# Performance work log

Hardware: AMD Instinct MI355X
Metric: run time of the kernel (lower is better)

The kernel has to match this reference:

```python
import jax, jax.numpy as jnp
import numpy as np


def setup_inputs() -> dict:
    key = jax.random.key(0)
    k1, k2, k3, k4 = jax.random.split(key, 4)
    B, T_dec, T_enc, H2 = 8, 64, 512, 512  # H2 = 2*hiddenSize
    encoderOutput = jax.random.normal(k1, (B, T_enc, H2), dtype=jnp.float32)
    decoderInput = jax.random.normal(k2, (B, T_dec, H2), dtype=jnp.float32)
    # fc: Linear(4H -> 2H); torch weight layout [out, in] = [2H, 4H]
    W = jax.random.normal(k3, (H2, 2 * H2), dtype=jnp.float32) * (1.0 / np.sqrt(2 * H2))
    b = jax.random.normal(k4, (H2,), dtype=jnp.float32) * 0.01
    return {"encoderOutput": encoderOutput, "decoderInput": decoderInput, "W": W, "b": b}


def reference(encoderOutput, decoderInput, W, b):
    # Original: for each (i, j), fc(cat(dec[:,i], enc[:,j])) then log_softmax over
    # the FEATURE dim (dim=1 of the flattened [-1, 2H] tensor), then
    # context[:, i] = sum_j log_softmax(...) * enc[:, j].
    H2 = encoderOutput.shape[-1]
    W_dec = W[:, :H2]   # columns multiplying the decoder half of the concat
    W_enc = W[:, H2:]   # columns multiplying the encoder half
    dec_part = jnp.einsum('bid,od->bio', decoderInput, W_dec)   # [B, T_dec, 2H]
    enc_part = jnp.einsum('bjd,od->bjo', encoderOutput, W_enc)  # [B, T_enc, 2H]
    logits = dec_part[:, :, None, :] + enc_part[:, None, :, :] + b  # [B, T_dec, T_enc, 2H]
    alpha = jax.nn.log_softmax(logits, axis=-1)  # softmax over feature dim, as in source
    context = jnp.einsum('bijd,bjd->bid', alpha, encoderOutput)  # [B, T_dec, 2H]
    return context
```

## Files before the change

kernel.cpp:

```cpp
#include <hip/hip_runtime.h>


namespace {
constexpr int kH  = 512;
constexpr int kTD = 64;
constexpr int kTE = 512;
constexpr int kB  = 8;
constexpr int kRD = kB * kTD;
constexpr int kRE = kB * kTE;
}

typedef __attribute__((ext_vector_type(8))) short short8;
typedef __attribute__((ext_vector_type(4))) float floatx4;

__device__ __forceinline__ unsigned short f2bf(float x) {
    unsigned u = __float_as_uint(x);
    u += 0x7fffu + ((u >> 16) & 1u);
    return (unsigned short)(u >> 16);
}
__device__ __forceinline__ float bf2f(unsigned short h) {
    return __uint_as_float(((unsigned)h) << 16);
}
__device__ __forceinline__ size_t fragTile(int rtile, int kt) {
    return ((size_t)rtile * 16 + kt) * 512;
}
__device__ __forceinline__ short8 pack8(float4 a, float4 b) {
    short8 r;
    r[0] = (short)f2bf(a.x); r[1] = (short)f2bf(a.y);
    r[2] = (short)f2bf(a.z); r[3] = (short)f2bf(a.w);
    r[4] = (short)f2bf(b.x); r[5] = (short)f2bf(b.y);
    r[6] = (short)f2bf(b.z); r[7] = (short)f2bf(b.w);
    return r;
}

__global__ __launch_bounds__(256) void fused_cast(
    const float* __restrict__ W, const float* __restrict__ dec,
    const float* __restrict__ enc,
    unsigned short* __restrict__ Wd_f, unsigned short* __restrict__ We_f,
    unsigned short* __restrict__ dec_f,
    unsigned short* __restrict__ enc_f, unsigned short* __restrict__ encT_f,
    float* __restrict__ S12)
{
    const int blk = blockIdx.x, t = threadIdx.x;
    const int w = t >> 6, l = t & 63;
    const int lr = l & 15, lc = l >> 4;
    if (blk < 256) {
        const int gw = blk * 4 + w;
        const int sel = gw >> 9, rem = gw & 511;
        const int ot = rem >> 4, kt = rem & 15;
        const int o = ot * 16 + lr;
        const float* src = W + (size_t)o * 1024 + sel * 512 + kt * 32 + lc * 8;
        const float4 v0 = *(const float4*)src;
        const float4 v1 = *(const float4*)(src + 4);
        unsigned short* dst = (sel ? We_f : Wd_f) + fragTile(ot, kt) + l * 8;
        *(short8*)dst = pack8(v0, v1);
        if (blk < 32) S12[blk * 256 + t] = 0.f;
    } else if (blk < 384) {
        const int gw = (blk - 256) * 4 + w;
        const int rt = gw >> 4, kt = gw & 15;
        const int r = rt * 16 + lr;
        const float* src = dec + (size_t)r * kH + kt * 32 + lc * 8;
        const float4 v0 = *(const float4*)src;
        const float4 v1 = *(const float4*)(src + 4);
        *(short8*)(dec_f + fragTile(rt, kt) + l * 8) = pack8(v0, v1);
    } else {
        __shared__ unsigned short s[64][36];
        const int e = blk - 384;
        const int kt = e & 15, jt = (e >> 4) & 7, b = e >> 7;
        const int j0 = jt * 64, d0 = kt * 32;
        const int jl = w * 16 + lr;
        const float* src = enc + ((size_t)(b * kTE + j0 + jl)) * kH + d0 + lc * 8;
        const float4 v0 = *(const float4*)src;
        const float4 v1 = *(const float4*)(src + 4);
        const short8 p = pack8(v0, v1);
        *(short8*)(enc_f + fragTile(b * 32 + jt * 4 + w, kt) + l * 8) = p;
#pragma unroll
        for (int i = 0; i < 8; ++i) s[jl][lc * 8 + i] = (unsigned short)p[i];
        __syncthreads();
        const int dt = w >> 1, jc = w & 1;
        const int dl = dt * 16 + lr;
        const int j8 = jc * 32 + lc * 8;
        short8 v;
#pragma unroll
        for (int i = 0; i < 8; ++i) v[i] = (short)s[j8 + i][dl];
        *(short8*)(encT_f + fragTile(b * 32 + kt * 2 + dt, jt * 2 + jc) + l * 8) = v;
    }
}

__global__ __launch_bounds__(256) void gemm1(
    const unsigned short* __restrict__ enc_f,
    const unsigned short* __restrict__ dec_f,
    const unsigned short* __restrict__ Wd_f,
    const unsigned short* __restrict__ We_f,
    const float* __restrict__ bias,
    const float* __restrict__ enc,
    unsigned short* __restrict__ part_bf, unsigned short* __restrict__ uv_f,
    float* __restrict__ S12)
{
    __shared__ float As[64][68];
    __shared__ float r1[16][68];
    __shared__ float r2[16][68];
    const int tile = blockIdx.x;
    const int ns = tile & 7, ms = tile >> 3;
    const int t = threadIdx.x, w = t >> 6, l = t & 63;
    const int qm = w >> 1, qn = w & 1;
    const bool isenc = (ms >= 8);
    const unsigned short* A = isenc ? enc_f : dec_f;
    const unsigned short* Bw = isenc ? We_f : Wd_f;
    const int art = (isenc ? (ms - 8) : ms) * 4 + qm * 2;
    const int brt = ns * 4 + qn * 2;

    floatx4 acc[2][2];
#pragma unroll
    for (int m = 0; m < 2; ++m)
#pragma unroll
        for (int n = 0; n < 2; ++n) acc[m][n] = (floatx4){0.f, 0.f, 0.f, 0.f};

    for (int kt = 0; kt < 16; ++kt) {
        short8 af[2], bfr[2];
#pragma unroll
        for (int m = 0; m < 2; ++m)
            af[m] = *(const short8*)(A + fragTile(art + m, kt) + l * 8);
#pragma unroll
        for (int n = 0; n < 2; ++n)
            bfr[n] = *(const short8*)(Bw + fragTile(brt + n, kt) + l * 8);
#pragma unroll
        for (int m = 0; m < 2; ++m)
#pragma unroll
            for (int n = 0; n < 2; ++n)
                acc[m][n] = __builtin_amdgcn_mfma_f32_16x16x32_bf16(af[m], bfr[n], acc[m][n], 0, 0, 0);
    }

    const int lr = l & 15, lq = l >> 4;
#pragma unroll
    for (int m = 0; m < 2; ++m)
#pragma unroll
        for (int n = 0; n < 2; ++n)
#pragma unroll
            for (int r = 0; r < 4; ++r)
                As[qm * 32 + m * 16 + lq * 4 + r][qn * 32 + n * 16 + lr] = acc[m][n][r];
    __syncthreads();

    const int rowbase = ms * 64, colbase = ns * 64;
    if (!isenc) {
#pragma unroll
        for (int h = 0; h < 2; ++h) {
            const int a = h * 256 + t;
            const int row = a >> 3, cc = (a & 7) * 8;
            const float4 v0 = *(const float4*)&As[row][cc];
            const float4 v1 = *(const float4*)&As[row][cc + 4];
            *(short8*)(part_bf + (size_t)(rowbase + row) * kH + colbase + cc) = pack8(v0, v1);
        }
    }
#pragma unroll
    for (int h = 0; h < 2; ++h) {
        const int s = h * 256 + t;
        const int rt = s >> 7, kc = (s >> 6) & 1, fl = s & 63;
        const int row = rt * 16 + (fl & 15);
        const int col = kc * 32 + (fl >> 4) * 8;
        const float4 v0 = *(const float4*)&As[row][col];
        const float4 v1 = *(const float4*)&As[row][col + 4];
        float4 b0 = make_float4(0.f, 0.f, 0.f, 0.f), b1 = b0;
        if (isenc) {
            b0 = *(const float4*)(bias + colbase + col);
            b1 = *(const float4*)(bias + colbase + col + 4);
        }
        short8 u;
        u[0] = (short)f2bf(__expf(v0.x + b0.x));
        u[1] = (short)f2bf(__expf(v0.y + b0.y));
        u[2] = (short)f2bf(__expf(v0.z + b0.z));
        u[3] = (short)f2bf(__expf(v0.w + b0.w));
        u[4] = (short)f2bf(__expf(v1.x + b1.x));
        u[5] = (short)f2bf(__expf(v1.y + b1.y));
        u[6] = (short)f2bf(__expf(v1.z + b1.z));
        u[7] = (short)f2bf(__expf(v1.w + b1.w));
        *(short8*)(uv_f + fragTile(ms * 4 + rt, ns * 2 + kc) + fl * 8) = u;
    }
    if (isenc) {
        const int b = (ms - 8) >> 3;
        const int jbase = ((ms - 8) & 7) * 64;
        const int o4 = (t & 15) * 4, jg = t >> 4;
        float4 s1p = make_float4(0.f, 0.f, 0.f, 0.f);
        float4 s2p = make_float4(0.f, 0.f, 0.f, 0.f);
#pragma unroll
        for (int jj = 0; jj < 4; ++jj) {
            const int j = jg * 4 + jj;
            const float4 ev = *(const float4*)(
                enc + ((size_t)(b * kTE + jbase + j)) * kH + colbase + o4);
            const float4 pv = *(const float4*)&As[j][o4];
            s1p.x += ev.x; s1p.y += ev.y; s1p.z += ev.z; s1p.w += ev.w;
            s2p.x = fmaf(pv.x, ev.x, s2p.x);
            s2p.y = fmaf(pv.y, ev.y, s2p.y);
            s2p.z = fmaf(pv.z, ev.z, s2p.z);
            s2p.w = fmaf(pv.w, ev.w, s2p.w);
        }
        *(float4*)&r1[jg][o4] = s1p;
        *(float4*)&r2[jg][o4] = s2p;
        __syncthreads();
        if (t < 64) {
            float a1 = 0.f, a2 = 0.f;
#pragma unroll
            for (int g = 0; g < 16; ++g) { a1 += r1[g][t]; a2 += r2[g][t]; }
            atomicAdd(&S12[b * kH + colbase + t], a1);
            atomicAdd(&S12[4096 + b * kH + colbase + t], a2);
        }
    }
}

__global__ __launch_bounds__(256) void lse_k(
    const unsigned short* __restrict__ uv_f, unsigned short* __restrict__ lse_f)
{
    __shared__ float red[4][16][68];
    const int blk = blockIdx.x, t = threadIdx.x;
    const int b = blk >> 5, rem = blk & 31;
    const int it = rem >> 3, jt = rem & 7;
    const int w = t >> 6, l = t & 63;
    const int art = b * 4 + it;
    const int vrt0 = 32 + b * 32 + jt * 4;

    floatx4 acc[4];
#pragma unroll
    for (int n = 0; n < 4; ++n) acc[n] = (floatx4){0.f, 0.f, 0.f, 0.f};
#pragma unroll
    for (int kk = 0; kk < 4; ++kk) {
        const int kt = w * 4 + kk;
        const short8 af = *(const short8*)(uv_f + fragTile(art, kt) + l * 8);
#pragma unroll
        for (int n = 0; n < 4; ++n)
            acc[n] = __builtin_amdgcn_mfma_f32_16x16x32_bf16(
                af, *(const short8*)(uv_f + fragTile(vrt0 + n, kt) + l * 8), acc[n], 0, 0, 0);
    }
    const int lr = l & 15, lq = l >> 4;
#pragma unroll
    for (int n = 0; n < 4; ++n)
#pragma unroll
        for (int r = 0; r < 4; ++r)
            red[w][lq * 4 + r][n * 16 + lr] = acc[n][r];
    __syncthreads();
    const int s = t >> 1, h = t & 1;
    const int kc = s >> 6, fl = s & 63;
    const int i = fl & 15;
    const int j = kc * 32 + (fl >> 4) * 8 + h * 4;
    float4 sum = *(const float4*)&red[0][i][j];
    const float4 s1 = *(const float4*)&red[1][i][j];
    const float4 s2 = *(const float4*)&red[2][i][j];
    const float4 s3 = *(const float4*)&red[3][i][j];
    sum.x += s1.x + s2.x + s3.x; sum.y += s1.y + s2.y + s3.y;
    sum.z += s1.z + s2.z + s3.z; sum.w += s1.w + s2.w + s3.w;
    ushort4 o;
    o.x = f2bf(__logf(sum.x)); o.y = f2bf(__logf(sum.y));
    o.z = f2bf(__logf(sum.z)); o.w = f2bf(__logf(sum.w));
    *(ushort4*)(lse_f + fragTile(b * 4 + it, jt * 2 + kc) + fl * 8 + h * 4) = o;
}

__global__ __launch_bounds__(256) void final_k(
    const unsigned short* __restrict__ lse_f,
    const unsigned short* __restrict__ encT_f,
    const unsigned short* __restrict__ part_bf,
    const float* __restrict__ bias,
    const float* __restrict__ S12,
    float* __restrict__ out)
{
    __shared__ float red[4][16][68];
    const int blk = blockIdx.x, t = threadIdx.x;
    const int b = blk >> 5, rem = blk & 31;
    const int it = rem >> 3, dt = rem & 7;
    const int w = t >> 6, l = t & 63;
    const int art = b * 4 + it;
    const int brt0 = b * 32 + dt * 4;

    floatx4 acc[4];
#pragma unroll
    for (int n = 0; n < 4; ++n) acc[n] = (floatx4){0.f, 0.f, 0.f, 0.f};
#pragma unroll
    for (int kk = 0; kk < 4; ++kk) {
        const int kt = w * 4 + kk;
        const short8 af = *(const short8*)(lse_f + fragTile(art, kt) + l * 8);
#pragma unroll
        for (int n = 0; n < 4; ++n)
            acc[n] = __builtin_amdgcn_mfma_f32_16x16x32_bf16(
                af, *(const short8*)(encT_f + fragTile(brt0 + n, kt) + l * 8), acc[n], 0, 0, 0);
    }
    const int lr = l & 15, lq = l >> 4;
#pragma unroll
    for (int n = 0; n < 4; ++n)
#pragma unroll
        for (int r = 0; r < 4; ++r)
            red[w][lq * 4 + r][n * 16 + lr] = acc[n][r];
    __syncthreads();
    const int i = t >> 4, d0 = (t & 15) * 4;
    float4 m = *(const float4*)&red[0][i][d0];
    const float4 m1 = *(const float4*)&red[1][i][d0];
    const float4 m2 = *(const float4*)&red[2][i][d0];
    const float4 m3 = *(const float4*)&red[3][i][d0];
    m.x += m1.x + m2.x + m3.x; m.y += m1.y + m2.y + m3.y;
    m.z += m1.z + m2.z + m3.z; m.w += m1.w + m2.w + m3.w;

    const int gd = dt * 64 + d0;
    const float4 s1 = *(const float4*)(S12 + b * kH + gd);
    const float4 s2 = *(const float4*)(S12 + 4096 + b * kH + gd);
    const float4 bi = *(const float4*)(bias + gd);
    const int row = b * kTD + it * 16 + i;
    const ushort4 dp = *(const ushort4*)(part_bf + (size_t)row * kH + gd);
    float4 o;
    o.x = fmaf(bf2f(dp.x) + bi.x, s1.x, s2.x) - m.x;
    o.y = fmaf(bf2f(dp.y) + bi.y, s1.y, s2.y) - m.y;
    o.z = fmaf(bf2f(dp.z) + bi.z, s1.z, s2.z) - m.z;
    o.w = fmaf(bf2f(dp.w) + bi.w, s1.w, s2.w) - m.w;
    *(float4*)(out + (size_t)row * kH + gd) = o;
}

extern "C" void kernel_launch(void* const* d_in, const int* in_sizes, int n_in,
                              void* d_out, int out_size, void* d_ws, size_t ws_size,
                              hipStream_t stream)
{
    (void)in_sizes; (void)n_in; (void)out_size; (void)ws_size;
    const float* enc  = (const float*)d_in[0];
    const float* dec  = (const float*)d_in[1];
    const float* W    = (const float*)d_in[2];
    const float* bias = (const float*)d_in[3];
    float* out = (float*)d_out;

    char* base = (char*)d_ws;
    unsigned short* part_bf = (unsigned short*)(base);
    unsigned short* uv_f    = (unsigned short*)(base + 4718592);
    unsigned short* enc_f   = (unsigned short*)(base + 9437184);
    unsigned short* encT_f  = (unsigned short*)(base + 13631488);
    unsigned short* dec_f   = (unsigned short*)(base + 17825792);
    unsigned short* Wd_f    = (unsigned short*)(base + 18350080);
    unsigned short* We_f    = (unsigned short*)(base + 18874368);
    unsigned short* lse_f   = (unsigned short*)(base + 19398656);
    float*          S12     = (float*)(base + 19922944);

    fused_cast<<<1408, 256, 0, stream>>>(W, dec, enc, Wd_f, We_f, dec_f,
                                         enc_f, encT_f, S12);
    gemm1<<<576, 256, 0, stream>>>(enc_f, dec_f, Wd_f, We_f, bias, enc,
                                   part_bf, uv_f, S12);
    lse_k<<<256, 256, 0, stream>>>(uv_f, lse_f);
    final_k<<<256, 256, 0, stream>>>(lse_f, encT_f, part_bf, bias, S12, out);
}
```

Measured before the change: 91.87 us.

## Merge four kernels into one cooperative persistent kernel with grid syncs

Replaces the four separate launches (cast, gemm1, lse, final) with a single cooperative kernel of 288 blocks that loops over the original block indices and separates the phases with grid-wide syncs. This removes three kernel launch gaps and their tail effects. The cost is fewer blocks than the original grids (1408 and 576), so each block does several units serially. The last two phases use only 256 of the 288 blocks, and grid.sync adds its own overhead.

Result: slower. 208.2 us (+126.7%).

```diff
diff --git a/kernel.cpp b/kernel.cpp
--- a/kernel.cpp
+++ b/kernel.cpp
@@ -1,4 +1,7 @@
 #include <hip/hip_runtime.h>
+#include <hip/hip_cooperative_groups.h>
+
+namespace cg = cooperative_groups;
 
 
 namespace {
@@ -7,7 +10,6 @@
 constexpr int kTE = 512;
 constexpr int kB  = 8;
 constexpr int kRD = kB * kTD;
-constexpr int kRE = kB * kTE;
 }
 
 typedef __attribute__((ext_vector_type(8))) short short8;
@@ -33,281 +35,271 @@
     return r;
 }
 
-__global__ __launch_bounds__(256) void fused_cast(
+__global__ void __launch_bounds__(256) mega(
     const float* __restrict__ W, const float* __restrict__ dec,
-    const float* __restrict__ enc,
+    const float* __restrict__ enc, const float* __restrict__ bias,
     unsigned short* __restrict__ Wd_f, unsigned short* __restrict__ We_f,
     unsigned short* __restrict__ dec_f,
     unsigned short* __restrict__ enc_f, unsigned short* __restrict__ encT_f,
-    float* __restrict__ S12)
+    unsigned short* __restrict__ part_bf, unsigned short* __restrict__ uv_f,
+    unsigned short* __restrict__ lse_f,
+    float* __restrict__ S12, float* __restrict__ out)
 {
-    const int blk = blockIdx.x, t = threadIdx.x;
-    const int w = t >> 6, l = t & 63;
+    cg::grid_group grid = cg::this_grid();
+    const int t = threadIdx.x, w = t >> 6, l = t & 63;
     const int lr = l & 15, lc = l >> 4;
-    if (blk < 256) {
-        const int gw = blk * 4 + w;
-        const int sel = gw >> 9, rem = gw & 511;
-        const int ot = rem >> 4, kt = rem & 15;
-        const int o = ot * 16 + lr;
-        const float* src = W + (size_t)o * 1024 + sel * 512 + kt * 32 + lc * 8;
-        const float4 v0 = *(const float4*)src;
-        const float4 v1 = *(const float4*)(src + 4);
-        unsigned short* dst = (sel ? We_f : Wd_f) + fragTile(ot, kt) + l * 8;
-        *(short8*)dst = pack8(v0, v1);
-        if (blk < 32) S12[blk * 256 + t] = 0.f;
-    } else if (blk < 384) {
-        const int gw = (blk - 256) * 4 + w;
-        const int rt = gw >> 4, kt = gw & 15;
-        const int r = rt * 16 + lr;
-        const float* src = dec + (size_t)r * kH + kt * 32 + lc * 8;
-        const float4 v0 = *(const float4*)src;
-        const float4 v1 = *(const float4*)(src + 4);
-        *(short8*)(dec_f + fragTile(rt, kt) + l * 8) = pack8(v0, v1);
-    } else {
-        __shared__ unsigned short s[64][36];
-        const int e = blk - 384;
-        const int kt = e & 15, jt = (e >> 4) & 7, b = e >> 7;
-        const int j0 = jt * 64, d0 = kt * 32;
-        const int jl = w * 16 + lr;
-        const float* src = enc + ((size_t)(b * kTE + j0 + jl)) * kH + d0 + lc * 8;
-        const float4 v0 = *(const float4*)src;
-        const float4 v1 = *(const float4*)(src + 4);
-        const short8 p = pack8(v0, v1);
-        *(short8*)(enc_f + fragTile(b * 32 + jt * 4 + w, kt) + l * 8) = p;
-#pragma unroll
-        for (int i = 0; i < 8; ++i) s[jl][lc * 8 + i] = (unsigned short)p[i];
-        __syncthreads();
-        const int dt = w >> 1, jc = w & 1;
-        const int dl = dt * 16 + lr;
-        const int j8 = jc * 32 + lc * 8;
-        short8 v;
-#pragma unroll
-        for (int i = 0; i < 8; ++i) v[i] = (short)s[j8 + i][dl];
-        *(short8*)(encT_f + fragTile(b * 32 + kt * 2 + dt, jt * 2 + jc) + l * 8) = v;
-    }
-}
-
-__global__ __launch_bounds__(256) void gemm1(
-    const unsigned short* __restrict__ enc_f,
-    const unsigned short* __restrict__ dec_f,
-    const unsigned short* __restrict__ Wd_f,
-    const unsigned short* __restrict__ We_f,
-    const float* __restrict__ bias,
-    const float* __restrict__ enc,
-    unsigned short* __restrict__ part_bf, unsigned short* __restrict__ uv_f,
-    float* __restrict__ S12)
-{
-    __shared__ float As[64][68];
-    __shared__ float r1[16][68];
-    __shared__ float r2[16][68];
-    const int tile = blockIdx.x;
-    const int ns = tile & 7, ms = tile >> 3;
-    const int t = threadIdx.x, w = t >> 6, l = t & 63;
-    const int qm = w >> 1, qn = w & 1;
-    const bool isenc = (ms >= 8);
-    const unsigned short* A = isenc ? enc_f : dec_f;
-    const unsigned short* Bw = isenc ? We_f : Wd_f;
-    const int art = (isenc ? (ms - 8) : ms) * 4 + qm * 2;
-    const int brt = ns * 4 + qn * 2;
-
-    floatx4 acc[2][2];
-#pragma unroll
-    for (int m = 0; m < 2; ++m)
-#pragma unroll
-        for (int n = 0; n < 2; ++n) acc[m][n] = (floatx4){0.f, 0.f, 0.f, 0.f};
-
-    for (int kt = 0; kt < 16; ++kt) {
-        short8 af[2], bfr[2];
-#pragma unroll
-        for (int m = 0; m < 2; ++m)
-            af[m] = *(const short8*)(A + fragTile(art + m, kt) + l * 8);
-#pragma unroll
-        for (int n = 0; n < 2; ++n)
-            bfr[n] = *(const short8*)(Bw + fragTile(brt + n, kt) + l * 8);
-#pragma unroll
-        for (int m = 0; m < 2; ++m)
-#pragma unroll
-            for (int n = 0; n < 2; ++n)
-                acc[m][n] = __builtin_amdgcn_mfma_f32_16x16x32_bf16(af[m], bfr[n], acc[m][n], 0, 0, 0);
-    }
-
-    const int lr = l & 15, lq = l >> 4;
-#pragma unroll
-    for (int m = 0; m < 2; ++m)
-#pragma unroll
-        for (int n = 0; n < 2; ++n)
-#pragma unroll
-            for (int r = 0; r < 4; ++r)
-                As[qm * 32 + m * 16 + lq * 4 + r][qn * 32 + n * 16 + lr] = acc[m][n][r];
-    __syncthreads();
-
-    const int rowbase = ms * 64, colbase = ns * 64;
-    if (!isenc) {
-#pragma unroll
-        for (int h = 0; h < 2; ++h) {
-            const int a = h * 256 + t;
-            const int row = a >> 3, cc = (a & 7) * 8;
-            const float4 v0 = *(const float4*)&As[row][cc];
-            const float4 v1 = *(const float4*)&As[row][cc + 4];
-            *(short8*)(part_bf + (size_t)(rowbase + row) * kH + colbase + cc) = pack8(v0, v1);
+    __shared__ __align__(16) char smem[26112];
+
+    for (int u = blockIdx.x; u < 1408; u += gridDim.x) {
+        if (u < 256) {
+            const int gw = u * 4 + w;
+            const int sel = gw >> 9, rem = gw & 511;
+            const int ot = rem >> 4, kt = rem & 15;
+            const int o = ot * 16 + lr;
+            const float* src = W + (size_t)o * 1024 + sel * 512 + kt * 32 + lc * 8;
+            const float4 v0 = *(const float4*)src;
+            const float4 v1 = *(const float4*)(src + 4);
+            unsigned short* dst = (sel ? We_f : Wd_f) + fragTile(ot, kt) + l * 8;
+            *(short8*)dst = pack8(v0, v1);
+            if (u < 32) S12[u * 256 + t] = 0.f;
+        } else if (u < 384) {
+            const int gw = (u - 256) * 4 + w;
+            const int rt = gw >> 4, kt = gw & 15;
+            const int r = rt * 16 + lr;
+            const float* src = dec + (size_t)r * kH + kt * 32 + lc * 8;
+            const float4 v0 = *(const float4*)src;
+            const float4 v1 = *(const float4*)(src + 4);
+            *(short8*)(dec_f + fragTile(rt, kt) + l * 8) = pack8(v0, v1);
+        } else {
+            unsigned short (*s)[36] = (unsigned short(*)[36])smem;
+            const int e = u - 384;
+            const int kt = e & 15, jt = (e >> 4) & 7, b = e >> 7;
+            const int j0 = jt * 64, d0 = kt * 32;
+            const int jl = w * 16 + lr;
+            const float* src = enc + ((size_t)(b * kTE + j0 + jl)) * kH + d0 + lc * 8;
+            const float4 v0 = *(const float4*)src;
+            const float4 v1 = *(const float4*)(src + 4);
+            const short8 p = pack8(v0, v1);
+            *(short8*)(enc_f + fragTile(b * 32 + jt * 4 + w, kt) + l * 8) = p;
+            __syncthreads();
+#pragma unroll
+            for (int i = 0; i < 8; ++i) s[jl][lc * 8 + i] = (unsigned short)p[i];
+            __syncthreads();
+            const int dt = w >> 1, jc = w & 1;
+            const int dl = dt * 16 + lr;
+            const int j8 = jc * 32 + lc * 8;
+            short8 v;
+#pragma unroll
+            for (int i = 0; i < 8; ++i) v[i] = (short)s[j8 + i][dl];
+            *(short8*)(encT_f + fragTile(b * 32 + kt * 2 + dt, jt * 2 + jc) + l * 8) = v;
         }
     }
-#pragma unroll
-    for (int h = 0; h < 2; ++h) {
-        const int s = h * 256 + t;
-        const int rt = s >> 7, kc = (s >> 6) & 1, fl = s & 63;
-        const int row = rt * 16 + (fl & 15);
-        const int col = kc * 32 + (fl >> 4) * 8;
-        const float4 v0 = *(const float4*)&As[row][col];
-        const float4 v1 = *(const float4*)&As[row][col + 4];
-        float4 b0 = make_float4(0.f, 0.f, 0.f, 0.f), b1 = b0;
-        if (isenc) {
-            b0 = *(const float4*)(bias + colbase + col);
-            b1 = *(const float4*)(bias + colbase + col + 4);
-        }
-        short8 u;
-        u[0] = (short)f2bf(__expf(v0.x + b0.x));
-        u[1] = (short)f2bf(__expf(v0.y + b0.y));
-        u[2] = (short)f2bf(__expf(v0.z + b0.z));
-        u[3] = (short)f2bf(__expf(v0.w + b0.w));
-        u[4] = (short)f2bf(__expf(v1.x + b1.x));
-        u[5] = (short)f2bf(__expf(v1.y + b1.y));
-        u[6] = (short)f2bf(__expf(v1.z + b1.z));
-        u[7] = (short)f2bf(__expf(v1.w + b1.w));
-        *(short8*)(uv_f + fragTile(ms * 4 + rt, ns * 2 + kc) + fl * 8) = u;
-    }
-    if (isenc) {
-        const int b = (ms - 8) >> 3;
-        const int jbase = ((ms - 8) & 7) * 64;
-        const int o4 = (t & 15) * 4, jg = t >> 4;
-        float4 s1p = make_float4(0.f, 0.f, 0.f, 0.f);
-        float4 s2p = make_float4(0.f, 0.f, 0.f, 0.f);
-#pragma unroll
-        for (int jj = 0; jj < 4; ++jj) {
-            const int j = jg * 4 + jj;
-            const float4 ev = *(const float4*)(
-                enc + ((size_t)(b * kTE + jbase + j)) * kH + colbase + o4);
-            const float4 pv = *(const float4*)&As[j][o4];
-            s1p.x += ev.x; s1p.y += ev.y; s1p.z += ev.z; s1p.w += ev.w;
-            s2p.x = fmaf(pv.x, ev.x, s2p.x);
-            s2p.y = fmaf(pv.y, ev.y, s2p.y);
-            s2p.z = fmaf(pv.z, ev.z, s2p.z);
-            s2p.w = fmaf(pv.w, ev.w, s2p.w);
-        }
-        *(float4*)&r1[jg][o4] = s1p;
-        *(float4*)&r2[jg][o4] = s2p;
-        __syncthreads();
-        if (t < 64) {
-            float a1 = 0.f, a2 = 0.f;
-#pragma unroll
-            for (int g = 0; g < 16; ++g) { a1 += r1[g][t]; a2 += r2[g][t]; }
-            atomicAdd(&S12[b * kH + colbase + t], a1);
-            atomicAdd(&S12[4096 + b * kH + colbase + t], a2);
+    grid.sync();
+
+    {
+        float (*As)[68] = (float(*)[68])smem;
+        float (*r1)[68] = (float(*)[68])(smem + 17408);
+        float (*r2)[68] = (float(*)[68])(smem + 21760);
+        const int qm = w >> 1, qn = w & 1;
+        for (int tile = blockIdx.x; tile < 576; tile += gridDim.x) {
+            const int ns = tile & 7, ms = tile >> 3;
+            const bool isenc = (ms >= 8);
+            const unsigned short* A = isenc ? enc_f : dec_f;
+            const unsigned short* Bw = isenc ? We_f : Wd_f;
+            const int art = (isenc ? (ms - 8) : ms) * 4 + qm * 2;
+            const int brt = ns * 4 + qn * 2;
+
+            floatx4 acc[2][2];
+#pragma unroll
+            for (int m = 0; m < 2; ++m)
+#pragma unroll
+                for (int n = 0; n < 2; ++n) acc[m][n] = (floatx4){0.f, 0.f, 0.f, 0.f};
+
+            for (int kt = 0; kt < 16; ++kt) {
+                short8 af[2], bfr[2];
+#pragma unroll
+                for (int m = 0; m < 2; ++m)
+                    af[m] = *(const short8*)(A + fragTile(art + m, kt) + l * 8);
+#pragma unroll
+                for (int n = 0; n < 2; ++n)
+                    bfr[n] = *(const short8*)(Bw + fragTile(brt + n, kt) + l * 8);
+#pragma unroll
+                for (int m = 0; m < 2; ++m)
+#pragma unroll
+                    for (int n = 0; n < 2; ++n)
+                        acc[m][n] = __builtin_amdgcn_mfma_f32_16x16x32_bf16(af[m], bfr[n], acc[m][n], 0, 0, 0);
+            }
+
+            __syncthreads();
+#pragma unroll
+            for (int m = 0; m < 2; ++m)
+#pragma unroll
+                for (int n = 0; n < 2; ++n)
+#pragma unroll
+                    for (int r = 0; r < 4; ++r)
+                        As[qm * 32 + m * 16 + (l >> 4) * 4 + r][qn * 32 + n * 16 + lr] = acc[m][n][r];
+            __syncthreads();
+
+            const int rowbase = ms * 64, colbase = ns * 64;
+            if (!isenc) {
+#pragma unroll
+                for (int h = 0; h < 2; ++h) {
+                    const int a = h * 256 + t;
+                    const int row = a >> 3, cc = (a & 7) * 8;
+                    const float4 v0 = *(const float4*)&As[row][cc];
+                    const float4 v1 = *(const float4*)&As[row][cc + 4];
+                    *(short8*)(part_bf + (size_t)(rowbase + row) * kH + colbase + cc) = pack8(v0, v1);
+                }
+            }
+#pragma unroll
+            for (int h = 0; h < 2; ++h) {
+                const int s = h * 256 + t;
+                const int rt = s >> 7, kc = (s >> 6) & 1, fl = s & 63;
+                const int row = rt * 16 + (fl & 15);
+                const int col = kc * 32 + (fl >> 4) * 8;
+                const float4 v0 = *(const float4*)&As[row][col];
+                const float4 v1 = *(const float4*)&As[row][col + 4];
+                float4 b0 = make_float4(0.f, 0.f, 0.f, 0.f), b1 = b0;
+                if (isenc) {
+                    b0 = *(const float4*)(bias + colbase + col);
+                    b1 = *(const float4*)(bias + colbase + col + 4);
+                }
+                short8 uu;
+                uu[0] = (short)f2bf(__expf(v0.x + b0.x));
+                uu[1] = (short)f2bf(__expf(v0.y + b0.y));
+                uu[2] = (short)f2bf(__expf(v0.z + b0.z));
+                uu[3] = (short)f2bf(__expf(v0.w + b0.w));
+                uu[4] = (short)f2bf(__expf(v1.x + b1.x));
+                uu[5] = (short)f2bf(__expf(v1.y + b1.y));
+                uu[6] = (short)f2bf(__expf(v1.z + b1.z));
+                uu[7] = (short)f2bf(__expf(v1.w + b1.w));
+                *(short8*)(uv_f + fragTile(ms * 4 + rt, ns * 2 + kc) + fl * 8) = uu;
+            }
+            if (isenc) {
+                const int b = (ms - 8) >> 3;
+                const int jbase = ((ms - 8) & 7) * 64;
+                const int o4 = (t & 15) * 4, jg = t >> 4;
+                float4 s1p = make_float4(0.f, 0.f, 0.f, 0.f);
+                float4 s2p = make_float4(0.f, 0.f, 0.f, 0.f);
+#pragma unroll
+                for (int jj = 0; jj < 4; ++jj) {
+                    const int j = jg * 4 + jj;
+                    const float4 ev = *(const float4*)(
+                        enc + ((size_t)(b * kTE + jbase + j)) * kH + colbase + o4);
+                    const float4 pv = *(const float4*)&As[j][o4];
+                    s1p.x += ev.x; s1p.y += ev.y; s1p.z += ev.z; s1p.w += ev.w;
+                    s2p.x = fmaf(pv.x, ev.x, s2p.x);
+                    s2p.y = fmaf(pv.y, ev.y, s2p.y);
+                    s2p.z = fmaf(pv.z, ev.z, s2p.z);
+                    s2p.w = fmaf(pv.w, ev.w, s2p.w);
+                }
+                *(float4*)&r1[jg][o4] = s1p;
+                *(float4*)&r2[jg][o4] = s2p;
+                __syncthreads();
+                if (t < 64) {
+                    float a1 = 0.f, a2 = 0.f;
+#pragma unroll
+                    for (int g = 0; g < 16; ++g) { a1 += r1[g][t]; a2 += r2[g][t]; }
+                    atomicAdd(&S12[b * kH + colbase + t], a1);
+                    atomicAdd(&S12[4096 + b * kH + colbase + t], a2);
+                }
+            }
         }
     }
-}
-
-__global__ __launch_bounds__(256) void lse_k(
-    const unsigned short* __restrict__ uv_f, unsigned short* __restrict__ lse_f)
-{
-    __shared__ float red[4][16][68];
-    const int blk = blockIdx.x, t = threadIdx.x;
-    const int b = blk >> 5, rem = blk & 31;
-    const int it = rem >> 3, jt = rem & 7;
-    const int w = t >> 6, l = t & 63;
-    const int art = b * 4 + it;
-    const int vrt0 = 32 + b * 32 + jt * 4;
-
-    floatx4 acc[4];
-#pragma unroll
-    for (int n = 0; n < 4; ++n) acc[n] = (floatx4){0.f, 0.f, 0.f, 0.f};
-#pragma unroll
-    for (int kk = 0; kk < 4; ++kk) {
-        const int kt = w * 4 + kk;
-        const short8 af = *(const short8*)(uv_f + fragTile(art, kt) + l * 8);
+    grid.sync();
+
+    if (blockIdx.x < 256) {
+        float (*red)[16][68] = (float(*)[16][68])smem;
+        const int blk = blockIdx.x;
+        const int b = blk >> 5, rem = blk & 31;
+        const int it = rem >> 3, jt = rem & 7;
+        const int art = b * 4 + it;
+        const int vrt0 = 32 + b * 32 + jt * 4;
+
+        floatx4 acc[4];
+#pragma unroll
+        for (int n = 0; n < 4; ++n) acc[n] = (floatx4){0.f, 0.f, 0.f, 0.f};
+#pragma unroll
+        for (int kk = 0; kk < 4; ++kk) {
+            const int kt = w * 4 + kk;
+            const short8 af = *(const short8*)(uv_f + fragTile(art, kt) + l * 8);
+#pragma unroll
+            for (int n = 0; n < 4; ++n)
+                acc[n] = __builtin_amdgcn_mfma_f32_16x16x32_bf16(
+                    af, *(const short8*)(uv_f + fragTile(vrt0 + n, kt) + l * 8), acc[n], 0, 0, 0);
+        }
+        const int lq = l >> 4;
 #pragma unroll
         for (int n = 0; n < 4; ++n)
-            acc[n] = __builtin_amdgcn_mfma_f32_16x16x32_bf16(
-                af, *(const short8*)(uv_f + fragTile(vrt0 + n, kt) + l * 8), acc[n], 0, 0, 0);
+#pragma unroll
+            for (int r = 0; r < 4; ++r)
+                red[w][lq * 4 + r][n * 16 + lr] = acc[n][r];
+        __syncthreads();
+        const int s = t >> 1, h = t & 1;
+        const int kc = s >> 6, fl = s & 63;
+        const int i = fl & 15;
+        const int j = kc * 32 + (fl >> 4) * 8 + h * 4;
+        float4 sum = *(const float4*)&red[0][i][j];
+        const float4 s1 = *(const float4*)&red[1][i][j];
+        const float4 s2 = *(const float4*)&red[2][i][j];
+        const float4 s3 = *(const float4*)&red[3][i][j];
+        sum.x += s1.x + s2.x + s3.x; sum.y += s1.y + s2.y + s3.y;
+        sum.z += s1.z + s2.z + s3.z; sum.w += s1.w + s2.w + s3.w;
+        ushort4 o;
+        o.x = f2bf(__logf(sum.x)); o.y = f2bf(__logf(sum.y));
+        o.z = f2bf(__logf(sum.z)); o.w = f2bf(__logf(sum.w));
+        *(ushort4*)(lse_f + fragTile(b * 4 + it, jt * 2 + kc) + fl * 8 + h * 4) = o;
     }
-    const int lr = l & 15, lq = l >> 4;
-#pragma unroll
-    for (int n = 0; n < 4; ++n)
-#pragma unroll
-        for (int r = 0; r < 4; ++r)
-            red[w][lq * 4 + r][n * 16 + lr] = acc[n][r];
-    __syncthreads();
-    const int s = t >> 1, h = t & 1;
-    const int kc = s >> 6, fl = s & 63;
-    const int i = fl & 15;
-    const int j = kc * 32 + (fl >> 4) * 8 + h * 4;
-    float4 sum = *(const float4*)&red[0][i][j];
-    const float4 s1 = *(const float4*)&red[1][i][j];
-    const float4 s2 = *(const float4*)&red[2][i][j];
-    const float4 s3 = *(const float4*)&red[3][i][j];
-    sum.x += s1.x + s2.x + s3.x; sum.y += s1.y + s2.y + s3.y;
-    sum.z += s1.z + s2.z + s3.z; sum.w += s1.w + s2.w + s3.w;
-    ushort4 o;
-    o.x = f2bf(__logf(sum.x)); o.y = f2bf(__logf(sum.y));
-    o.z = f2bf(__logf(sum.z)); o.w = f2bf(__logf(sum.w));
-    *(ushort4*)(lse_f + fragTile(b * 4 + it, jt * 2 + kc) + fl * 8 + h * 4) = o;
-}
-
-__global__ __launch_bounds__(256) void final_k(
-    const unsigned short* __restrict__ lse_f,
-    const unsigned short* __restrict__ encT_f,
-    const unsigned short* __restrict__ part_bf,
-    const float* __restrict__ bias,
-    const float* __restrict__ S12,
-    float* __restrict__ out)
-{
-    __shared__ float red[4][16][68];
-    const int blk = blockIdx.x, t = threadIdx.x;
-    const int b = blk >> 5, rem = blk & 31;
-    const int it = rem >> 3, dt = rem & 7;
-    const int w = t >> 6, l = t & 63;
-    const int art = b * 4 + it;
-    const int brt0 = b * 32 + dt * 4;
-
-    floatx4 acc[4];
-#pragma unroll
-    for (int n = 0; n < 4; ++n) acc[n] = (floatx4){0.f, 0.f, 0.f, 0.f};
-#pragma unroll
-    for (int kk = 0; kk < 4; ++kk) {
-        const int kt = w * 4 + kk;
-        const short8 af = *(const short8*)(lse_f + fragTile(art, kt) + l * 8);
+    grid.sync();
+
+    if (blockIdx.x < 256) {
+        float (*red)[16][68] = (float(*)[16][68])smem;
+        const int blk = blockIdx.x;
+        const int b = blk >> 5, rem = blk & 31;
+        const int it = rem >> 3, dt = rem & 7;
+        const int art = b * 4 + it;
+        const int brt0 = b * 32 + dt * 4;
+
+        floatx4 acc[4];
+#pragma unroll
+        for (int n = 0; n < 4; ++n) acc[n] = (floatx4){0.f, 0.f, 0.f, 0.f};
+#pragma unroll
+        for (int kk = 0; kk < 4; ++kk) {
+            const int kt = w * 4 + kk;
+            const short8 af = *(const short8*)(lse_f + fragTile(art, kt) + l * 8);
+#pragma unroll
+            for (int n = 0; n < 4; ++n)
+                acc[n] = __builtin_amdgcn_mfma_f32_16x16x32_bf16(
+                    af, *(const short8*)(encT_f + fragTile(brt0 + n, kt) + l * 8), acc[n], 0, 0, 0);
+        }
+        const int lq = l >> 4;
 #pragma unroll
         for (int n = 0; n < 4; ++n)
-            acc[n] = __builtin_amdgcn_mfma_f32_16x16x32_bf16(
-                af, *(const short8*)(encT_f + fragTile(brt0 + n, kt) + l * 8), acc[n], 0, 0, 0);
+#pragma unroll
+            for (int r = 0; r < 4; ++r)
+                red[w][lq * 4 + r][n * 16 + lr] = acc[n][r];
+        __syncthreads();
+        const int i = t >> 4, d0 = (t & 15) * 4;
+        float4 m = *(const float4*)&red[0][i][d0];
+        const float4 m1 = *(const float4*)&red[1][i][d0];
+        const float4 m2 = *(const float4*)&red[2][i][d0];
+        const float4 m3 = *(const float4*)&red[3][i][d0];
+        m.x += m1.x + m2.x + m3.x; m.y += m1.y + m2.y + m3.y;
+        m.z += m1.z + m2.z + m3.z; m.w += m1.w + m2.w + m3.w;
+
+        const int gd = dt * 64 + d0;
+        const float4 s1 = *(const float4*)(S12 + b * kH + gd);
+        const float4 s2 = *(const float4*)(S12 + 4096 + b * kH + gd);
+        const float4 bi = *(const float4*)(bias + gd);
+        const int row = b * kTD + it * 16 + i;
+        const ushort4 dp = *(const ushort4*)(part_bf + (size_t)row * kH + gd);
+        float4 o;
+        o.x = fmaf(bf2f(dp.x) + bi.x, s1.x, s2.x) - m.x;
+        o.y = fmaf(bf2f(dp.y) + bi.y, s1.y, s2.y) - m.y;
+        o.z = fmaf(bf2f(dp.z) + bi.z, s1.z, s2.z) - m.z;
+        o.w = fmaf(bf2f(dp.w) + bi.w, s1.w, s2.w) - m.w;
+        *(float4*)(out + (size_t)row * kH + gd) = o;
     }
-    const int lr = l & 15, lq = l >> 4;
-#pragma unroll
-    for (int n = 0; n < 4; ++n)
-#pragma unroll
-        for (int r = 0; r < 4; ++r)
-            red[w][lq * 4 + r][n * 16 + lr] = acc[n][r];
-    __syncthreads();
-    const int i = t >> 4, d0 = (t & 15) * 4;
-    float4 m = *(const float4*)&red[0][i][d0];
-    const float4 m1 = *(const float4*)&red[1][i][d0];
-    const float4 m2 = *(const float4*)&red[2][i][d0];
-    const float4 m3 = *(const float4*)&red[3][i][d0];
-    m.x += m1.x + m2.x + m3.x; m.y += m1.y + m2.y + m3.y;
-    m.z += m1.z + m2.z + m3.z; m.w += m1.w + m2.w + m3.w;
-
-    const int gd = dt * 64 + d0;
-    const float4 s1 = *(const float4*)(S12 + b * kH + gd);
-    const float4 s2 = *(const float4*)(S12 + 4096 + b * kH + gd);
-    const float4 bi = *(const float4*)(bias + gd);
-    const int row = b * kTD + it * 16 + i;
-    const ushort4 dp = *(const ushort4*)(part_bf + (size_t)row * kH + gd);
-    float4 o;
-    o.x = fmaf(bf2f(dp.x) + bi.x, s1.x, s2.x) - m.x;
-    o.y = fmaf(bf2f(dp.y) + bi.y, s1.y, s2.y) - m.y;
-    o.z = fmaf(bf2f(dp.z) + bi.z, s1.z, s2.z) - m.z;
-    o.w = fmaf(bf2f(dp.w) + bi.w, s1.w, s2.w) - m.w;
-    *(float4*)(out + (size_t)row * kH + gd) = o;
 }
 
 extern "C" void kernel_launch(void* const* d_in, const int* in_sizes, int n_in,
@@ -332,10 +324,11 @@
     unsigned short* lse_f   = (unsigned short*)(base + 19398656);
     float*          S12     = (float*)(base + 19922944);
 
-    fused_cast<<<1408, 256, 0, stream>>>(W, dec, enc, Wd_f, We_f, dec_f,
-                                         enc_f, encT_f, S12);
-    gemm1<<<576, 256, 0, stream>>>(enc_f, dec_f, Wd_f, We_f, bias, enc,
-                                   part_bf, uv_f, S12);
-    lse_k<<<256, 256, 0, stream>>>(uv_f, lse_f);
-    final_k<<<256, 256, 0, stream>>>(lse_f, encT_f, part_bf, bias, S12, out);
-}
+    void* args[] = {
+        (void*)&W, (void*)&dec, (void*)&enc, (void*)&bias,
+        (void*)&Wd_f, (void*)&We_f, (void*)&dec_f, (void*)&enc_f, (void*)&encT_f,
+        (void*)&part_bf, (void*)&uv_f, (void*)&lse_f, (void*)&S12, (void*)&out
+    };
+    hipLaunchCooperativeKernel((const void*)mega, dim3(288), dim3(256),
+                               args, 0, stream);
+}
```

## Fuse LSE GEMM into final kernel and coarsen encoder cast blocks

Applied to the files above, without the earlier changes.

Merges the log-sum-exp GEMM into the final context kernel. Each block now computes its full 16x512 LSE tile into shared memory and uses it directly, which removes one launch and the global lse round trip. The trade-off is that each LSE tile is recomputed by all 8 dt blocks, so that GEMM does 8x more MFMA work and reads more of uv_f. The encoder cast/transpose path also gives each block 8 k-tiles instead of 1, cutting that launch's grid from 1408 to 512 blocks at the cost of an extra barrier per iteration.

After: 117.0 us. +27.4%, slower.

```diff
diff --git a/kernel.cpp b/kernel.cpp
--- a/kernel.cpp
+++ b/kernel.cpp
@@ -7,7 +7,6 @@
 constexpr int kTE = 512;
 constexpr int kB  = 8;
 constexpr int kRD = kB * kTD;
-constexpr int kRE = kB * kTE;
 }
 
 typedef __attribute__((ext_vector_type(8))) short short8;
@@ -66,24 +65,29 @@
     } else {
         __shared__ unsigned short s[64][36];
         const int e = blk - 384;
-        const int kt = e & 15, jt = (e >> 4) & 7, b = e >> 7;
-        const int j0 = jt * 64, d0 = kt * 32;
+        const int b = e >> 4, sub = e & 15;
+        const int jt = sub >> 1, kh = sub & 1;
+        const int j0 = jt * 64;
         const int jl = w * 16 + lr;
-        const float* src = enc + ((size_t)(b * kTE + j0 + jl)) * kH + d0 + lc * 8;
-        const float4 v0 = *(const float4*)src;
-        const float4 v1 = *(const float4*)(src + 4);
-        const short8 p = pack8(v0, v1);
-        *(short8*)(enc_f + fragTile(b * 32 + jt * 4 + w, kt) + l * 8) = p;
-#pragma unroll
-        for (int i = 0; i < 8; ++i) s[jl][lc * 8 + i] = (unsigned short)p[i];
-        __syncthreads();
-        const int dt = w >> 1, jc = w & 1;
-        const int dl = dt * 16 + lr;
-        const int j8 = jc * 32 + lc * 8;
-        short8 v;
-#pragma unroll
-        for (int i = 0; i < 8; ++i) v[i] = (short)s[j8 + i][dl];
-        *(short8*)(encT_f + fragTile(b * 32 + kt * 2 + dt, jt * 2 + jc) + l * 8) = v;
+        for (int kt = kh * 8; kt < kh * 8 + 8; ++kt) {
+            const int d0 = kt * 32;
+            const float* src = enc + ((size_t)(b * kTE + j0 + jl)) * kH + d0 + lc * 8;
+            const float4 v0 = *(const float4*)src;
+            const float4 v1 = *(const float4*)(src + 4);
+            const short8 p = pack8(v0, v1);
+            *(short8*)(enc_f + fragTile(b * 32 + jt * 4 + w, kt) + l * 8) = p;
+            __syncthreads();
+#pragma unroll
+            for (int i = 0; i < 8; ++i) s[jl][lc * 8 + i] = (unsigned short)p[i];
+            __syncthreads();
+            const int dt2 = w >> 1, jc = w & 1;
+            const int dl = dt2 * 16 + lr;
+            const int j8 = jc * 32 + lc * 8;
+            short8 v;
+#pragma unroll
+            for (int i = 0; i < 8; ++i) v[i] = (short)s[j8 + i][dl];
+            *(short8*)(encT_f + fragTile(b * 32 + kt * 2 + dt2, jt * 2 + jc) + l * 8) = v;
+        }
     }
 }
 
@@ -207,81 +211,57 @@
     }
 }
 
-__global__ __launch_bounds__(256) void lse_k(
-    const unsigned short* __restrict__ uv_f, unsigned short* __restrict__ lse_f)
-{
-    __shared__ float red[4][16][68];
-    const int blk = blockIdx.x, t = threadIdx.x;
-    const int b = blk >> 5, rem = blk & 31;
-    const int it = rem >> 3, jt = rem & 7;
-    const int w = t >> 6, l = t & 63;
-    const int art = b * 4 + it;
-    const int vrt0 = 32 + b * 32 + jt * 4;
-
-    floatx4 acc[4];
-#pragma unroll
-    for (int n = 0; n < 4; ++n) acc[n] = (floatx4){0.f, 0.f, 0.f, 0.f};
-#pragma unroll
-    for (int kk = 0; kk < 4; ++kk) {
-        const int kt = w * 4 + kk;
-        const short8 af = *(const short8*)(uv_f + fragTile(art, kt) + l * 8);
-#pragma unroll
-        for (int n = 0; n < 4; ++n)
-            acc[n] = __builtin_amdgcn_mfma_f32_16x16x32_bf16(
-                af, *(const short8*)(uv_f + fragTile(vrt0 + n, kt) + l * 8), acc[n], 0, 0, 0);
-    }
-    const int lr = l & 15, lq = l >> 4;
-#pragma unroll
-    for (int n = 0; n < 4; ++n)
-#pragma unroll
-        for (int r = 0; r < 4; ++r)
-            red[w][lq * 4 + r][n * 16 + lr] = acc[n][r];
-    __syncthreads();
-    const int s = t >> 1, h = t & 1;
-    const int kc = s >> 6, fl = s & 63;
-    const int i = fl & 15;
-    const int j = kc * 32 + (fl >> 4) * 8 + h * 4;
-    float4 sum = *(const float4*)&red[0][i][j];
-    const float4 s1 = *(const float4*)&red[1][i][j];
-    const float4 s2 = *(const float4*)&red[2][i][j];
-    const float4 s3 = *(const float4*)&red[3][i][j];
-    sum.x += s1.x + s2.x + s3.x; sum.y += s1.y + s2.y + s3.y;
-    sum.z += s1.z + s2.z + s3.z; sum.w += s1.w + s2.w + s3.w;
-    ushort4 o;
-    o.x = f2bf(__logf(sum.x)); o.y = f2bf(__logf(sum.y));
-    o.z = f2bf(__logf(sum.z)); o.w = f2bf(__logf(sum.w));
-    *(ushort4*)(lse_f + fragTile(b * 4 + it, jt * 2 + kc) + fl * 8 + h * 4) = o;
-}
-
-__global__ __launch_bounds__(256) void final_k(
-    const unsigned short* __restrict__ lse_f,
+__global__ __launch_bounds__(256) void final2(
+    const unsigned short* __restrict__ uv_f,
     const unsigned short* __restrict__ encT_f,
     const unsigned short* __restrict__ part_bf,
     const float* __restrict__ bias,
     const float* __restrict__ S12,
     float* __restrict__ out)
 {
+    __shared__ unsigned short lse_lds[8192];
     __shared__ float red[4][16][68];
     const int blk = blockIdx.x, t = threadIdx.x;
-    const int b = blk >> 5, rem = blk & 31;
-    const int it = rem >> 3, dt = rem & 7;
+    const int b = blk >> 5, it = (blk >> 3) & 3, dt = blk & 7;
     const int w = t >> 6, l = t & 63;
+    const int lr = l & 15, lq = l >> 4;
+
     const int art = b * 4 + it;
+    floatx4 accA[8];
+#pragma unroll
+    for (int n = 0; n < 8; ++n) accA[n] = (floatx4){0.f, 0.f, 0.f, 0.f};
+    for (int kt = 0; kt < 16; ++kt) {
+        const short8 af = *(const short8*)(uv_f + fragTile(art, kt) + l * 8);
+#pragma unroll
+        for (int n = 0; n < 8; ++n)
+            accA[n] = __builtin_amdgcn_mfma_f32_16x16x32_bf16(
+                af, *(const short8*)(uv_f + fragTile(32 + b * 32 + w * 8 + n, kt) + l * 8),
+                accA[n], 0, 0, 0);
+    }
+#pragma unroll
+    for (int n = 0; n < 8; ++n)
+#pragma unroll
+        for (int r = 0; r < 4; ++r) {
+            const int i = lq * 4 + r;
+            const int jl = w * 128 + n * 16 + lr;
+            lse_lds[(jl >> 5) * 512 + i * 8 + ((jl >> 3) & 3) * 128 + (jl & 7)] =
+                f2bf(__logf(accA[n][r]));
+        }
+    __syncthreads();
+
     const int brt0 = b * 32 + dt * 4;
-
     floatx4 acc[4];
 #pragma unroll
     for (int n = 0; n < 4; ++n) acc[n] = (floatx4){0.f, 0.f, 0.f, 0.f};
 #pragma unroll
     for (int kk = 0; kk < 4; ++kk) {
         const int kt = w * 4 + kk;
-        const short8 af = *(const short8*)(lse_f + fragTile(art, kt) + l * 8);
+        const short8 af = *(const short8*)(lse_lds + kt * 512 + l * 8);
 #pragma unroll
         for (int n = 0; n < 4; ++n)
             acc[n] = __builtin_amdgcn_mfma_f32_16x16x32_bf16(
                 af, *(const short8*)(encT_f + fragTile(brt0 + n, kt) + l * 8), acc[n], 0, 0, 0);
     }
-    const int lr = l & 15, lq = l >> 4;
 #pragma unroll
     for (int n = 0; n < 4; ++n)
 #pragma unroll
@@ -329,13 +309,11 @@
     unsigned short* dec_f   = (unsigned short*)(base + 17825792);
     unsigned short* Wd_f    = (unsigned short*)(base + 18350080);
     unsigned short* We_f    = (unsigned short*)(base + 18874368);
-    unsigned short* lse_f   = (unsigned short*)(base + 19398656);
     float*          S12     = (float*)(base + 19922944);
 
-    fused_cast<<<1408, 256, 0, stream>>>(W, dec, enc, Wd_f, We_f, dec_f,
-                                         enc_f, encT_f, S12);
+    fused_cast<<<512, 256, 0, stream>>>(W, dec, enc, Wd_f, We_f, dec_f,
+                                        enc_f, encT_f, S12);
     gemm1<<<576, 256, 0, stream>>>(enc_f, dec_f, Wd_f, We_f, bias, enc,
                                    part_bf, uv_f, S12);
-    lse_k<<<256, 256, 0, stream>>>(uv_f, lse_f);
-    final_k<<<256, 256, 0, stream>>>(lse_f, encT_f, part_bf, bias, S12, out);
-}
+    final2<<<256, 256, 0, stream>>>(uv_f, encT_f, part_bf, bias, S12, out);
+}
```
